# Kernel optimization log

Measured on AMD Instinct MI355X. Metric: run time of the kernel, lower is better.

Reference implementation:

```python
import jax, jax.numpy as jnp
import numpy as np

L, D, F, H = 6, 512, 2048, 8
DH = D // H
SCALE = DH ** -0.5
B, S = 2, 2048


def _ln(x, w, b):
    m = jnp.mean(x, axis=-1, keepdims=True)
    v = jnp.var(x, axis=-1, keepdims=True)
    return (x - m) * jax.lax.rsqrt(v + 1e-5) * w + b


def setup_inputs() -> dict:
    key = jax.random.key(0)
    ks = jax.random.split(key, 10)
    s = 0.02
    return {
        "x": jax.random.normal(ks[0], (B, S, D), jnp.float32),
        "mask": jnp.zeros((B, 1, 1, S), jnp.float32),
        "ln1_w": jnp.ones((L, D), jnp.float32),
        "ln1_b": jnp.zeros((L, D), jnp.float32),
        "in_w": s * jax.random.normal(ks[1], (L, D, 3 * D), jnp.float32),
        "in_b": jnp.zeros((L, 3 * D), jnp.float32),
        "out_w": s * jax.random.normal(ks[2], (L, D, D), jnp.float32),
        "out_b": jnp.zeros((L, D), jnp.float32),
        "ln2_w": jnp.ones((L, D), jnp.float32),
        "ln2_b": jnp.zeros((L, D), jnp.float32),
        "ffn1_w": s * jax.random.normal(ks[3], (L, D, F), jnp.float32),
        "ffn1_b": jnp.zeros((L, F), jnp.float32),
        "ffn2_w": s * jax.random.normal(ks[4], (L, F, D), jnp.float32),
        "ffn2_b": jnp.zeros((L, D), jnp.float32),
        "norm_w": jnp.ones((D,), jnp.float32),
        "norm_b": jnp.zeros((D,), jnp.float32),
    }


def reference(x, mask, ln1_w, ln1_b, in_w, in_b, out_w, out_b,
              ln2_w, ln2_b, ffn1_w, ffn1_b, ffn2_w, ffn2_b, norm_w, norm_b):
    def step(h, p):
        (l1w, l1b, iw, ib, ow, ob, l2w, l2b, f1w, f1b, f2w, f2b) = p
        # --- self-attention (pre-norm) ---
        y = _ln(h, l1w, l1b)
        proj = y @ iw + ib                       # [B,S,3D]
        q, k, v = jnp.split(proj, 3, axis=-1)    # each [B,S,D]
        q = q.reshape(B, S, H, DH)
        k = k.reshape(B, S, H, DH)
        v = v.reshape(B, S, H, DH)
        dot = jnp.einsum('bqhd,bkhd->bhqk', q * SCALE, k) + mask  # [B,H,S,S]
        att = jax.nn.softmax(dot, axis=-1)
        o = jnp.einsum('bhqk,bkhd->bqhd', att, v).reshape(B, S, D)
        h = o @ ow + ob + h
        # --- FFN (pre-norm) ---
        y = _ln(h, l2w, l2b)
        y = jax.nn.relu(y @ f1w + f1b) @ f2w + f2b
        return h + y, None

    params = (ln1_w, ln1_b, in_w, in_b, out_w, out_b,
              ln2_w, ln2_b, ffn1_w, ffn1_b, ffn2_w, ffn2_b)
    x, _ = jax.lax.scan(step, x, params)
    return _ln(x, norm_w, norm_b)
```

## Files before the change

### kernel.cpp

```cpp
#include <hip/hip_runtime.h>
#include <hip/hip_bf16.h>
#include <stdint.h>


typedef __bf16 bf16x8 __attribute__((ext_vector_type(8)));
typedef __bf16 bf16x4 __attribute__((ext_vector_type(4)));
typedef float f32x4 __attribute__((ext_vector_type(4)));
typedef unsigned short u16;
typedef unsigned short u16x8 __attribute__((ext_vector_type(8)));

#define NB 2
#define NS 2048
#define ND 512
#define NH 8
#define NDH 64
#define NF 2048
#define NL 6
#define NCHUNK 4
#define CK (NS / NCHUNK)
#define LOG2E 1.4426950408889634f
#define QSCALE (0.125f * LOG2E)

#if defined(__has_builtin)
#if __has_builtin(__builtin_amdgcn_global_load_lds)
#define HAVE_GLDS 1
#endif
#endif
#ifndef HAVE_GLDS
#define HAVE_GLDS 0
#endif

#if HAVE_GLDS
__device__ __forceinline__ void glds16(const u16* g, u16* l) {
  __builtin_amdgcn_global_load_lds(
      (const __attribute__((address_space(1))) unsigned int*)g,
      (__attribute__((address_space(3))) unsigned int*)l, 16, 0, 0);
}
#endif

__device__ __forceinline__ u16 f2bf(float f) {
  unsigned u = __float_as_uint(f);
  u += 0x7FFFu + ((u >> 16) & 1u);
  return (u16)(u >> 16);
}

__device__ __forceinline__ int xswz(int w, int n) {
  return (w & 7) * (n >> 3) + (w >> 3);
}

__global__ __launch_bounds__(256) void wcvt_t(const float* __restrict__ src,
                                              u16* __restrict__ dst,
                                              int K, int N) {
  __shared__ float tile[32][33];
  int l = blockIdx.z;
  const float* s = src + (size_t)l * K * N;
  u16* d = dst + (size_t)l * K * N;
  int k0 = blockIdx.y * 32, n0 = blockIdx.x * 32;
  int tx = threadIdx.x, ty = threadIdx.y;
  for (int i = 0; i < 32; i += 8)
    tile[ty + i][tx] = s[(size_t)(k0 + ty + i) * N + n0 + tx];
  __syncthreads();
  for (int i = 0; i < 32; i += 8)
    d[(size_t)(n0 + ty + i) * K + k0 + tx] = f2bf(tile[tx][ty + i]);
}

template <int OUT_BF16>
__global__ __launch_bounds__(256) void ln_k(const float* __restrict__ x,
                                            const float* __restrict__ w,
                                            const float* __restrict__ b,
                                            void* __restrict__ out) {
  int row = blockIdx.x;
  int t = threadIdx.x;
  const float* xr = x + (size_t)row * ND;
  float2 v = ((const float2*)xr)[t];
  float s = v.x + v.y, ss = v.x * v.x + v.y * v.y;
  for (int o = 32; o > 0; o >>= 1) {
    s += __shfl_down(s, o);
    ss += __shfl_down(ss, o);
  }
  __shared__ float rs[4], rss[4];
  if ((t & 63) == 0) { rs[t >> 6] = s; rss[t >> 6] = ss; }
  __syncthreads();
  float S = rs[0] + rs[1] + rs[2] + rs[3];
  float SS = rss[0] + rss[1] + rss[2] + rss[3];
  float mean = S * (1.0f / ND);
  float var = SS * (1.0f / ND) - mean * mean;
  float rstd = rsqrtf(var + 1e-5f);
  float2 wv = ((const float2*)w)[t];
  float2 bv = ((const float2*)b)[t];
  float y0 = (v.x - mean) * rstd * wv.x + bv.x;
  float y1 = (v.y - mean) * rstd * wv.y + bv.y;
  if (OUT_BF16) {
    ushort2 p; p.x = f2bf(y0); p.y = f2bf(y1);
    ((ushort2*)out)[(size_t)row * (ND / 2) + t] = p;
  } else {
    float2 p; p.x = y0; p.y = y1;
    ((float2*)out)[(size_t)row * (ND / 2) + t] = p;
  }
}

template <int EPI, int BM, int BN, int BK>
__device__ __forceinline__ void gemm_body(int flat, int gx, int gy,
                                          const u16* __restrict__ A,
                                          const u16* __restrict__ Bt,
                                          const float* __restrict__ bias,
                                          const float* __restrict__ resid,
                                          void* __restrict__ C,
                                          int M, int N, int K, int lda,
                                          u16* sm) {
  constexpr int MT = BM / 32;
  constexpr int NT = BN / 32;
  constexpr int CB = BK / 8;
  constexpr int RPP = 2048 / BK;
  constexpr int AP = BM / RPP;
  constexpr int BP = BN / RPP;
  constexpr int KK = BK / 32;
  constexpr int LAU = BM * BK;
  constexpr int LBU = BN * BK;
  int s_id = xswz(flat, gx * gy);
  int bn = s_id % gx, bm = s_id / gx;
  int t = threadIdx.x;
  int wave = t >> 6, lane = t & 63, quad = lane >> 4, l15 = lane & 15;
  int wm = (wave >> 1) * (BM / 2), wn = (wave & 1) * (BN / 2);
  f32x4 acc[MT][NT] = {};
  int srow = t / CB;
  int scol = ((t % CB) ^ (srow & (CB - 1))) * 8;
  const u16* Ag = A + (size_t)(bm * BM) * lda;
  const u16* Bg = Bt + (size_t)(bn * BN) * lda;

  auto stage = [&](int k0, int buf) {
    u16* laB = sm + buf * LAU;
    u16* lbB = sm + 2 * LAU + buf * LBU;
#if HAVE_GLDS
    u16* laW = laB + wave * 512;
    u16* lbW = lbB + wave * 512;
#pragma unroll
    for (int g = 0; g < AP; g++)
      glds16(&Ag[(size_t)(srow + g * RPP) * lda + k0 + scol], laW + g * 2048);
#pragma unroll
    for (int g = 0; g < BP; g++)
      glds16(&Bg[(size_t)(srow + g * RPP) * lda + k0 + scol], lbW + g * 2048);
#else
#pragma unroll
    for (int g = 0; g < AP; g++)
      *(bf16x8*)&laB[(srow + g * RPP) * BK + (t % CB) * 8] =
          *(const bf16x8*)&Ag[(size_t)(srow + g * RPP) * lda + k0 + scol];
#pragma unroll
    for (int g = 0; g < BP; g++)
      *(bf16x8*)&lbB[(srow + g * RPP) * BK + (t % CB) * 8] =
          *(const bf16x8*)&Bg[(size_t)(srow + g * RPP) * lda + k0 + scol];
#endif
  };

  stage(0, 0);
  const int nk = K / BK;
  int cur = 0;
  for (int ks = 0; ks < nk; ks++) {
    __syncthreads();
    if (ks + 1 < nk) stage((ks + 1) * BK, cur ^ 1);
    const u16* lac = sm + cur * LAU;
    const u16* lbc = sm + 2 * LAU + cur * LBU;
#pragma unroll
    for (int kk = 0; kk < KK; kk++) {
      bf16x8 af[MT], bfr[NT];
#pragma unroll
      for (int i = 0; i < MT; i++) {
        int row = wm + i * 16 + l15;
        af[i] = *(const bf16x8*)&lac[row * BK + ((kk * 4 + quad) ^ (row & (CB - 1))) * 8];
      }
#pragma unroll
      for (int i = 0; i < NT; i++) {
        int row = wn + i * 16 + l15;
        bfr[i] = *(const bf16x8*)&lbc[row * BK + ((kk * 4 + quad) ^ (row & (CB - 1))) * 8];
      }
#pragma unroll
      for (int mt = 0; mt < MT; mt++)
#pragma unroll
        for (int nt = 0; nt < NT; nt++)
          acc[mt][nt] = __builtin_amdgcn_mfma_f32_16x16x32_bf16(
              af[mt], bfr[nt], acc[mt][nt], 0, 0, 0);
    }
    cur ^= 1;
  }
#pragma unroll
  for (int mt = 0; mt < MT; mt++)
#pragma unroll
    for (int nt = 0; nt < NT; nt++) {
      int col = bn * BN + wn + nt * 16 + l15;
      float bcol = (EPI == 3) ? 0.f : bias[col];
#pragma unroll
      for (int r = 0; r < 4; r++) {
        int row = bm * BM + wm + mt * 16 + quad * 4 + r;
        float v = acc[mt][nt][r] + ((EPI == 3) ? bias[row] : bcol);
        if (EPI == 1) v = fmaxf(v, 0.f);
        if (EPI == 2)
          ((float*)C)[(size_t)row * N + col] = v + resid[(size_t)row * N + col];
        else
          ((u16*)C)[(size_t)row * N + col] = f2bf(v);
      }
    }
}

template <int EPI, int BM, int BN, int BK>
__global__ __launch_bounds__(256) void gemm_bt(const u16* __restrict__ A,
                                               const u16* __restrict__ Bt,
                                               const float* __restrict__ bias,
                                               const float* __restrict__ resid,
                                               void* __restrict__ C,
                                               int M, int N, int K, int lda) {
  __shared__ __align__(16) u16 sm[2 * BM * BK + 2 * BN * BK];
  int flat = blockIdx.x + gridDim.x * blockIdx.y;
  gemm_body<EPI, BM, BN, BK>(flat, gridDim.x, gridDim.y, A, Bt, bias, resid,
                             C, M, N, K, lda, sm);
}

__global__ __launch_bounds__(256) void qkv_k(const u16* __restrict__ ybuf,
                                             const u16* __restrict__ wq_l,
                                             const float* __restrict__ inb_l,
                                             u16* __restrict__ qk,
                                             u16* __restrict__ vtb) {
  __shared__ __align__(16) u16 sm[32768];
  int f = blockIdx.x;
  if (f < 512) {
    gemm_body<0, 64, 128, 64>(f, 2 * ND / 128, NB * NS / 64, ybuf, wq_l,
                              inb_l, nullptr, qk, NB * NS, 2 * ND, ND, ND, sm);
  } else {
    gemm_body<3, 64, 64, 128>(f - 512, NB * NS / 64, ND / 64,
                              wq_l + (size_t)2 * ND * ND, ybuf,
                              inb_l + 2 * ND, nullptr, vtb, ND, NB * NS, ND,
                              ND, sm);
  }
}

__global__ __launch_bounds__(512) void attn_k(const u16* __restrict__ qk,
                                              const u16* __restrict__ vt,
                                              const float* __restrict__ mask,
                                              u16* __restrict__ opart,
                                              float* __restrict__ lbuf) {
  __shared__ u16 kt_s[64 * 64];
  __shared__ u16 vt_s[64 * 64];
  __shared__ u16 p_s[8][16 * 64];
  __shared__ float mask_s[CK];
  int flat = blockIdx.x + 16 * (blockIdx.y + 16 * blockIdx.z);
  int s_id = xswz(flat, 16 * 16 * NCHUNK);
  int qt = s_id & 15;
  int bh = (s_id >> 4) & 15;
  int c = s_id >> 8;
  int b = bh >> 3, h = bh & 7;
  int t = threadIdx.x;
  int wave = t >> 6, lane = t & 63, quad = lane >> 4, l15 = lane & 15;

  {
    const float* mrow = mask + b * NS + c * CK;
    mask_s[t] = mrow[t] * LOG2E;
  }

  int qrow = qt * 128 + wave * 16 + l15;
  const u16* qbase = qk + ((size_t)(b * NS + qrow)) * (2 * ND) + h * NDH;
  bf16x8 qf[2];
  qf[0] = *(const bf16x8*)&qbase[quad * 8];
  qf[1] = *(const bf16x8*)&qbase[32 + quad * 8];
#pragma unroll
  for (int e = 0; e < 8; e++) {
    qf[0][e] = (__bf16)((float)qf[0][e] * QSCALE);
    qf[1][e] = (__bf16)((float)qf[1][e] * QSCALE);
  }
  bf16x8 ones;
#pragma unroll
  for (int e = 0; e < 8; e++) ones[e] = (__bf16)1.0f;

  f32x4 oacc[4] = {};
  f32x4 ls = {};

  int srow8 = t >> 3;
  int segsw = ((t & 7) ^ ((t >> 3) & 7)) * 8;
  const u16* kg0 = qk + ((size_t)(b * NS + srow8)) * (2 * ND) + ND + h * NDH + segsw;
  const u16* vg0 = vt + ((size_t)(h * NDH + srow8)) * (NB * NS) + b * NS + segsw;
#if HAVE_GLDS
  u16* ktB = kt_s + wave * 512;
  u16* vtB = vt_s + wave * 512;
#endif
  u16* pw = &p_s[wave][0];
  int l7 = l15 & 7;
  for (int kt0 = c * CK; kt0 < (c + 1) * CK; kt0 += 64) {
    __syncthreads();
#if HAVE_GLDS
    glds16(&kg0[(size_t)kt0 * (2 * ND)], ktB);
    glds16(&vg0[kt0], vtB);
#else
    *(bf16x8*)&kt_s[srow8 * 64 + (t & 7) * 8] =
        *(const bf16x8*)&kg0[(size_t)kt0 * (2 * ND)];
    *(bf16x8*)&vt_s[srow8 * 64 + (t & 7) * 8] = *(const bf16x8*)&vg0[kt0];
#endif
    __syncthreads();
    int ktl = kt0 - c * CK;
    f32x4 sc[4];
#pragma unroll
    for (int nt = 0; nt < 4; nt++)
      sc[nt] = *(const f32x4*)&mask_s[ktl + nt * 16 + quad * 4];
#pragma unroll
    for (int nt = 0; nt < 4; nt++) {
      int row = nt * 16 + l15;
      bf16x8 kf0 = *(const bf16x8*)&kt_s[row * 64 + (quad ^ (row & 7)) * 8];
      bf16x8 kf1 = *(const bf16x8*)&kt_s[row * 64 + ((quad + 4) ^ (row & 7)) * 8];
      sc[nt] = __builtin_amdgcn_mfma_f32_16x16x32_bf16(kf0, qf[0], sc[nt], 0, 0, 0);
      sc[nt] = __builtin_amdgcn_mfma_f32_16x16x32_bf16(kf1, qf[1], sc[nt], 0, 0, 0);
    }
#pragma unroll
    for (int nt = 0; nt < 4; nt++) {
      float2 plo, phi;
      plo.x = __builtin_amdgcn_exp2f(sc[nt][0]);
      plo.y = __builtin_amdgcn_exp2f(sc[nt][1]);
      phi.x = __builtin_amdgcn_exp2f(sc[nt][2]);
      phi.y = __builtin_amdgcn_exp2f(sc[nt][3]);
      __hip_bfloat162 b01 = __float22bfloat162_rn(plo);
      __hip_bfloat162 b23 = __float22bfloat162_rn(phi);
      uint2 pk;
      pk.x = *reinterpret_cast<unsigned int*>(&b01);
      pk.y = *reinterpret_cast<unsigned int*>(&b23);
      int cb = nt * 2 + (quad >> 1);
      int col = ((cb ^ l7) << 3) + (quad & 1) * 4;
      *reinterpret_cast<uint2*>(&pw[l15 * 64 + col]) = pk;
    }
    asm volatile("s_waitcnt lgkmcnt(0)" ::: "memory");
#pragma unroll
    for (int kk = 0; kk < 2; kk++) {
      int cbr = kk * 4 + quad;
      bf16x8 pf = *(const bf16x8*)&pw[l15 * 64 + ((cbr ^ l7) << 3)];
#pragma unroll
      for (int nt = 0; nt < 4; nt++) {
        int row = nt * 16 + l15;
        bf16x8 vf = *(const bf16x8*)&vt_s[row * 64 + ((kk * 4 + quad) ^ (row & 7)) * 8];
        oacc[nt] = __builtin_amdgcn_mfma_f32_16x16x32_bf16(pf, vf, oacc[nt], 0, 0, 0);
      }
      ls = __builtin_amdgcn_mfma_f32_16x16x32_bf16(pf, ones, ls, 0, 0, 0);
    }
  }
  u16* ob = opart + (((size_t)(c * NB * NH + bh) * NS) + qt * 128 + wave * 16) * NDH;
#pragma unroll
  for (int nt = 0; nt < 4; nt++)
#pragma unroll
    for (int r = 0; r < 4; r++)
      ob[(size_t)(quad * 4 + r) * NDH + nt * 16 + l15] = f2bf(oacc[nt][r]);
  if (l15 == 0) {
    size_t li = (size_t)(c * NB * NH + bh) * NS + qt * 128 + wave * 16 + quad * 4;
#pragma unroll
    for (int r = 0; r < 4; r++) lbuf[li + r] = ls[r];
  }
}

__global__ __launch_bounds__(256) void attn_merge(const u16* __restrict__ opart,
                                                  const float* __restrict__ lbuf,
                                                  u16* __restrict__ o) {
  int gt = blockIdx.x * 256 + threadIdx.x;
  int grp = gt & 7;
  int s = (gt >> 3) & (NS - 1);
  int bh = gt >> 14;
  float L = 0.f;
#pragma unroll
  for (int c = 0; c < NCHUNK; c++)
    L += lbuf[(size_t)(c * NB * NH + bh) * NS + s];
  float inv = 1.0f / L;
  float acc[8] = {};
#pragma unroll
  for (int c = 0; c < NCHUNK; c++) {
    bf16x8 ov = *(const bf16x8*)&opart[((size_t)(c * NB * NH + bh) * NS + s) * NDH + grp * 8];
#pragma unroll
    for (int j = 0; j < 8; j++) acc[j] += (float)ov[j];
  }
  u16x8 res;
#pragma unroll
  for (int j = 0; j < 8; j++) res[j] = f2bf(acc[j] * inv);
  int b = bh >> 3, h = bh & 7;
  *(u16x8*)&o[((size_t)(b * NS + s)) * ND + h * NDH + grp * 8] = res;
}

extern "C" void kernel_launch(void* const* d_in, const int* in_sizes, int n_in,
                              void* d_out, int out_size, void* d_ws, size_t ws_size,
                              hipStream_t stream) {
  const float* x = (const float*)d_in[0];
  const float* mask = (const float*)d_in[1];
  const float* ln1w = (const float*)d_in[2];
  const float* ln1b = (const float*)d_in[3];
  const float* in_w = (const float*)d_in[4];
  const float* in_b = (const float*)d_in[5];
  const float* out_w = (const float*)d_in[6];
  const float* out_b = (const float*)d_in[7];
  const float* ln2w = (const float*)d_in[8];
  const float* ln2b = (const float*)d_in[9];
  const float* f1w = (const float*)d_in[10];
  const float* f1b = (const float*)d_in[11];
  const float* f2w = (const float*)d_in[12];
  const float* f2b = (const float*)d_in[13];
  const float* normw = (const float*)d_in[14];
  const float* normb = (const float*)d_in[15];

  char* ws = (char*)d_ws;
  auto carve = [&](size_t bytes) {
    char* p = ws;
    ws += (bytes + 255) & ~(size_t)255;
    return p;
  };
  u16* wq_t = (u16*)carve((size_t)NL * 3 * ND * ND * 2);
  u16* wo_t = (u16*)carve((size_t)NL * ND * ND * 2);
  u16* w1_t = (u16*)carve((size_t)NL * NF * ND * 2);
  u16* w2_t = (u16*)carve((size_t)NL * ND * NF * 2);
  u16* ybuf = (u16*)carve((size_t)NB * NS * ND * 2);
  u16* qk = (u16*)carve((size_t)NB * NS * 2 * ND * 2);
  u16* vtb = (u16*)carve((size_t)ND * NB * NS * 2);
  u16* obuf = (u16*)carve((size_t)NB * NS * ND * 2);
  u16* ubuf = (u16*)carve((size_t)NB * NS * NF * 2);
  float* hA = (float*)carve((size_t)NB * NS * ND * 4);
  float* hB = (float*)carve((size_t)NB * NS * ND * 4);
  float* lbuf = (float*)carve((size_t)NCHUNK * NB * NH * NS * 4);
  u16* opart = ubuf;

  const int M = NB * NS;
  dim3 tb(32, 8);
  wcvt_t<<<dim3(3 * ND / 32, ND / 32, NL), tb, 0, stream>>>(in_w, wq_t, ND, 3 * ND);
  wcvt_t<<<dim3(ND / 32, ND / 32, NL), tb, 0, stream>>>(out_w, wo_t, ND, ND);
  wcvt_t<<<dim3(NF / 32, ND / 32, NL), tb, 0, stream>>>(f1w, w1_t, ND, NF);
  wcvt_t<<<dim3(ND / 32, NF / 32, NL), tb, 0, stream>>>(f2w, w2_t, NF, ND);

  const float* hin = x;
  for (int l = 0; l < NL; l++) {
    ln_k<1><<<M, 256, 0, stream>>>(hin, ln1w + l * ND, ln1b + l * ND, ybuf);
    qkv_k<<<1024, 256, 0, stream>>>(ybuf, wq_t + (size_t)l * 3 * ND * ND,
                                    in_b + (size_t)l * 3 * ND, qk, vtb);
    attn_k<<<dim3(NS / 128, NB * NH, NCHUNK), 512, 0, stream>>>(
        qk, vtb, mask, opart, lbuf);
    attn_merge<<<(NB * NH * NS * 8) / 256, 256, 0, stream>>>(opart, lbuf, obuf);
    gemm_bt<2, 64, 64, 128><<<dim3(ND / 64, M / 64), 256, 0, stream>>>(
        obuf, wo_t + (size_t)l * ND * ND, out_b + l * ND, hin, hB, M, ND, ND, ND);
    ln_k<1><<<M, 256, 0, stream>>>(hB, ln2w + l * ND, ln2b + l * ND, ybuf);
    gemm_bt<1, 128, 128, 64><<<dim3(NF / 128, M / 128), 256, 0, stream>>>(
        ybuf, w1_t + (size_t)l * NF * ND, f1b + l * NF, nullptr, ubuf,
        M, NF, ND, ND);
    gemm_bt<2, 64, 64, 128><<<dim3(ND / 64, M / 64), 256, 0, stream>>>(
        ubuf, w2_t + (size_t)l * ND * NF, f2b + l * ND, hB, hA, M, ND, NF, NF);
    hin = hA;
  }
  ln_k<0><<<M, 256, 0, stream>>>(hA, normw, normb, (float*)d_out);
}
```

Before: 717.8 us.

## Rewrite attention with 32x32x16 MFMA, register-resident P, 4 waves per block

Reworks the attention kernel to use 32x32x16 bf16 MFMA tiles with each wave owning 32 query rows, and cuts blocks from 8 waves to 4. The P matrix is now rearranged in registers using cross-half lane shuffles instead of round-tripping through shared memory. The row sum is accumulated in scalar registers rather than through an extra MFMA against a vector of ones. This is meant to remove the LDS writes, reads and waits for P and the wasted ones-MFMA, at the cost of more registers per lane and fewer waves per block to hide latency.

```diff
diff --git a/kernel.cpp b/kernel.cpp
--- a/kernel.cpp
+++ b/kernel.cpp
@@ -6,6 +6,7 @@
 typedef __bf16 bf16x8 __attribute__((ext_vector_type(8)));
 typedef __bf16 bf16x4 __attribute__((ext_vector_type(4)));
 typedef float f32x4 __attribute__((ext_vector_type(4)));
+typedef float f32x16 __attribute__((ext_vector_type(16)));
 typedef unsigned short u16;
 typedef unsigned short u16x8 __attribute__((ext_vector_type(8)));
 
@@ -232,14 +233,13 @@
   }
 }
 
-__global__ __launch_bounds__(512) void attn_k(const u16* __restrict__ qk,
+__global__ __launch_bounds__(256) void attn_k(const u16* __restrict__ qk,
                                               const u16* __restrict__ vt,
                                               const float* __restrict__ mask,
                                               u16* __restrict__ opart,
                                               float* __restrict__ lbuf) {
   __shared__ u16 kt_s[64 * 64];
   __shared__ u16 vt_s[64 * 64];
-  __shared__ u16 p_s[8][16 * 64];
   __shared__ float mask_s[CK];
   int flat = blockIdx.x + 16 * (blockIdx.y + 16 * blockIdx.z);
   int s_id = xswz(flat, 16 * 16 * NCHUNK);
@@ -248,29 +248,27 @@
   int c = s_id >> 8;
   int b = bh >> 3, h = bh & 7;
   int t = threadIdx.x;
-  int wave = t >> 6, lane = t & 63, quad = lane >> 4, l15 = lane & 15;
+  int wave = t >> 6, lane = t & 63, l31 = lane & 31, H = lane >> 5;
+  bool H0 = (H == 0);
 
   {
     const float* mrow = mask + b * NS + c * CK;
     mask_s[t] = mrow[t] * LOG2E;
-  }
-
-  int qrow = qt * 128 + wave * 16 + l15;
+    mask_s[t + 256] = mrow[t + 256] * LOG2E;
+  }
+
+  int qrow = qt * 128 + wave * 32 + l31;
   const u16* qbase = qk + ((size_t)(b * NS + qrow)) * (2 * ND) + h * NDH;
-  bf16x8 qf[2];
-  qf[0] = *(const bf16x8*)&qbase[quad * 8];
-  qf[1] = *(const bf16x8*)&qbase[32 + quad * 8];
-#pragma unroll
-  for (int e = 0; e < 8; e++) {
-    qf[0][e] = (__bf16)((float)qf[0][e] * QSCALE);
-    qf[1][e] = (__bf16)((float)qf[1][e] * QSCALE);
-  }
-  bf16x8 ones;
-#pragma unroll
-  for (int e = 0; e < 8; e++) ones[e] = (__bf16)1.0f;
-
-  f32x4 oacc[4] = {};
-  f32x4 ls = {};
+  bf16x8 qf[4];
+#pragma unroll
+  for (int kk = 0; kk < 4; kk++) {
+    qf[kk] = *(const bf16x8*)&qbase[kk * 16 + H * 8];
+#pragma unroll
+    for (int e = 0; e < 8; e++) qf[kk][e] = (__bf16)((float)qf[kk][e] * QSCALE);
+  }
+
+  f32x16 oacc[2] = {};
+  float lhalf = 0.f;
 
   int srow8 = t >> 3;
   int segsw = ((t & 7) ^ ((t >> 3) & 7)) * 8;
@@ -280,72 +278,92 @@
   u16* ktB = kt_s + wave * 512;
   u16* vtB = vt_s + wave * 512;
 #endif
-  u16* pw = &p_s[wave][0];
-  int l7 = l15 & 7;
   for (int kt0 = c * CK; kt0 < (c + 1) * CK; kt0 += 64) {
     __syncthreads();
 #if HAVE_GLDS
     glds16(&kg0[(size_t)kt0 * (2 * ND)], ktB);
+    glds16(&kg0[(size_t)(kt0 + 32) * (2 * ND)], ktB + 2048);
     glds16(&vg0[kt0], vtB);
+    glds16(&vg0[kt0 + (size_t)32 * (NB * NS)], vtB + 2048);
 #else
     *(bf16x8*)&kt_s[srow8 * 64 + (t & 7) * 8] =
         *(const bf16x8*)&kg0[(size_t)kt0 * (2 * ND)];
+    *(bf16x8*)&kt_s[(srow8 + 32) * 64 + (t & 7) * 8] =
+        *(const bf16x8*)&kg0[(size_t)(kt0 + 32) * (2 * ND)];
     *(bf16x8*)&vt_s[srow8 * 64 + (t & 7) * 8] = *(const bf16x8*)&vg0[kt0];
+    *(bf16x8*)&vt_s[(srow8 + 32) * 64 + (t & 7) * 8] =
+        *(const bf16x8*)&vg0[kt0 + (size_t)32 * (NB * NS)];
 #endif
     __syncthreads();
     int ktl = kt0 - c * CK;
-    f32x4 sc[4];
-#pragma unroll
-    for (int nt = 0; nt < 4; nt++)
-      sc[nt] = *(const f32x4*)&mask_s[ktl + nt * 16 + quad * 4];
-#pragma unroll
-    for (int nt = 0; nt < 4; nt++) {
-      int row = nt * 16 + l15;
-      bf16x8 kf0 = *(const bf16x8*)&kt_s[row * 64 + (quad ^ (row & 7)) * 8];
-      bf16x8 kf1 = *(const bf16x8*)&kt_s[row * 64 + ((quad + 4) ^ (row & 7)) * 8];
-      sc[nt] = __builtin_amdgcn_mfma_f32_16x16x32_bf16(kf0, qf[0], sc[nt], 0, 0, 0);
-      sc[nt] = __builtin_amdgcn_mfma_f32_16x16x32_bf16(kf1, qf[1], sc[nt], 0, 0, 0);
-    }
-#pragma unroll
-    for (int nt = 0; nt < 4; nt++) {
-      float2 plo, phi;
-      plo.x = __builtin_amdgcn_exp2f(sc[nt][0]);
-      plo.y = __builtin_amdgcn_exp2f(sc[nt][1]);
-      phi.x = __builtin_amdgcn_exp2f(sc[nt][2]);
-      phi.y = __builtin_amdgcn_exp2f(sc[nt][3]);
-      __hip_bfloat162 b01 = __float22bfloat162_rn(plo);
-      __hip_bfloat162 b23 = __float22bfloat162_rn(phi);
-      uint2 pk;
-      pk.x = *reinterpret_cast<unsigned int*>(&b01);
-      pk.y = *reinterpret_cast<unsigned int*>(&b23);
-      int cb = nt * 2 + (quad >> 1);
-      int col = ((cb ^ l7) << 3) + (quad & 1) * 4;
-      *reinterpret_cast<uint2*>(&pw[l15 * 64 + col]) = pk;
-    }
-    asm volatile("s_waitcnt lgkmcnt(0)" ::: "memory");
-#pragma unroll
-    for (int kk = 0; kk < 2; kk++) {
-      int cbr = kk * 4 + quad;
-      bf16x8 pf = *(const bf16x8*)&pw[l15 * 64 + ((cbr ^ l7) << 3)];
-#pragma unroll
-      for (int nt = 0; nt < 4; nt++) {
-        int row = nt * 16 + l15;
-        bf16x8 vf = *(const bf16x8*)&vt_s[row * 64 + ((kk * 4 + quad) ^ (row & 7)) * 8];
-        oacc[nt] = __builtin_amdgcn_mfma_f32_16x16x32_bf16(pf, vf, oacc[nt], 0, 0, 0);
-      }
-      ls = __builtin_amdgcn_mfma_f32_16x16x32_bf16(pf, ones, ls, 0, 0, 0);
-    }
-  }
-  u16* ob = opart + (((size_t)(c * NB * NH + bh) * NS) + qt * 128 + wave * 16) * NDH;
-#pragma unroll
-  for (int nt = 0; nt < 4; nt++)
-#pragma unroll
-    for (int r = 0; r < 4; r++)
-      ob[(size_t)(quad * 4 + r) * NDH + nt * 16 + l15] = f2bf(oacc[nt][r]);
-  if (l15 == 0) {
-    size_t li = (size_t)(c * NB * NH + bh) * NS + qt * 128 + wave * 16 + quad * 4;
-#pragma unroll
-    for (int r = 0; r < 4; r++) lbuf[li + r] = ls[r];
+    f32x16 sc[2];
+#pragma unroll
+    for (int kt = 0; kt < 2; kt++) {
+#pragma unroll
+      for (int g = 0; g < 4; g++) {
+        f32x4 mm = *(const f32x4*)&mask_s[ktl + 32 * kt + 8 * g + 4 * H];
+#pragma unroll
+        for (int e = 0; e < 4; e++) sc[kt][4 * g + e] = mm[e];
+      }
+      int row = 32 * kt + l31;
+#pragma unroll
+      for (int kk = 0; kk < 4; kk++) {
+        bf16x8 kf = *(const bf16x8*)&kt_s[row * 64 + (((2 * kk + H) ^ (row & 7)) << 3)];
+        sc[kt] = __builtin_amdgcn_mfma_f32_32x32x16_bf16(kf, qf[kk], sc[kt], 0, 0, 0);
+      }
+    }
+    unsigned p2[2][4][2];
+#pragma unroll
+    for (int kt = 0; kt < 2; kt++)
+#pragma unroll
+      for (int r2 = 0; r2 < 4; r2++)
+#pragma unroll
+        for (int p = 0; p < 2; p++) {
+          float e0 = __builtin_amdgcn_exp2f(sc[kt][4 * r2 + 2 * p]);
+          float e1 = __builtin_amdgcn_exp2f(sc[kt][4 * r2 + 2 * p + 1]);
+          lhalf += e0 + e1;
+          float2 pp; pp.x = e0; pp.y = e1;
+          __hip_bfloat162 bb = __float22bfloat162_rn(pp);
+          p2[kt][r2][p] = *reinterpret_cast<unsigned*>(&bb);
+        }
+    bf16x8 pfk[4];
+#pragma unroll
+    for (int kk = 0; kk < 4; kk++) {
+      const int kt = kk >> 1;
+      const int b0 = 2 * (kk & 1), b1 = b0 + 1;
+      unsigned sent0 = H0 ? p2[kt][b1][0] : p2[kt][b0][0];
+      unsigned sent1 = H0 ? p2[kt][b1][1] : p2[kt][b0][1];
+      unsigned r0 = (unsigned)__shfl_xor((int)sent0, 32);
+      unsigned r1 = (unsigned)__shfl_xor((int)sent1, 32);
+      uint4 pk;
+      pk.x = H0 ? p2[kt][b0][0] : r0;
+      pk.y = H0 ? p2[kt][b0][1] : r1;
+      pk.z = H0 ? r0 : p2[kt][b1][0];
+      pk.w = H0 ? r1 : p2[kt][b1][1];
+      pfk[kk] = *reinterpret_cast<bf16x8*>(&pk);
+    }
+#pragma unroll
+    for (int dt = 0; dt < 2; dt++) {
+      int row = dt * 32 + l31;
+#pragma unroll
+      for (int kk = 0; kk < 4; kk++) {
+        bf16x8 vf = *(const bf16x8*)&vt_s[row * 64 + (((2 * kk + H) ^ (row & 7)) << 3)];
+        oacc[dt] = __builtin_amdgcn_mfma_f32_32x32x16_bf16(pfk[kk], vf, oacc[dt], 0, 0, 0);
+      }
+    }
+  }
+  float lsum = lhalf + (float)__shfl_xor((float)lhalf, 32);
+  u16* ob = opart + (((size_t)(c * NB * NH + bh) * NS) + qt * 128 + wave * 32) * NDH;
+#pragma unroll
+  for (int dt = 0; dt < 2; dt++)
+#pragma unroll
+    for (int r = 0; r < 16; r++) {
+      int q = (r & 3) + 8 * (r >> 2) + 4 * H;
+      ob[(size_t)q * NDH + dt * 32 + l31] = f2bf(oacc[dt][r]);
+    }
+  if (H == 0) {
+    size_t li = (size_t)(c * NB * NH + bh) * NS + qt * 128 + wave * 32 + l31;
+    lbuf[li] = lsum;
   }
 }
 
@@ -427,7 +445,7 @@
     ln_k<1><<<M, 256, 0, stream>>>(hin, ln1w + l * ND, ln1b + l * ND, ybuf);
     qkv_k<<<1024, 256, 0, stream>>>(ybuf, wq_t + (size_t)l * 3 * ND * ND,
                                     in_b + (size_t)l * 3 * ND, qk, vtb);
-    attn_k<<<dim3(NS / 128, NB * NH, NCHUNK), 512, 0, stream>>>(
+    attn_k<<<dim3(NS / 128, NB * NH, NCHUNK), 256, 0, stream>>>(
         qk, vtb, mask, opart, lbuf);
     attn_merge<<<(NB * NH * NS * 8) / 256, 256, 0, stream>>>(opart, lbuf, obuf);
     gemm_bt<2, 64, 64, 128><<<dim3(ND / 64, M / 64), 256, 0, stream>>>(
```

New measurement: 708.5 us. No clear change (-1.3%).
